# Kernel optimization log

Measured on AMD Instinct MI355X. Metric: run time of the kernel, lower is better.

## Reference

```python
import jax, jax.numpy as jnp
import numpy as np

EPS_LN = 1e-5   # torch.nn.LayerNorm default eps
EPS_Q = 1e-5    # BitNetQuantizer eps
QMAX = 127.0    # 2**(8-1) - 1 for 8-bit activations


def _layernorm(v):
    # LayerNorm without affine params, biased variance (torch default)
    mu = jnp.mean(v, axis=-1, keepdims=True)
    var = jnp.var(v, axis=-1, keepdims=True)
    return (v - mu) / jnp.sqrt(var + EPS_LN)


def setup_inputs() -> dict:
    key = jax.random.key(0)
    k1, k2, k3 = jax.random.split(key, 3)
    B, S, DIN, DOUT = 4, 4096, 2048, 2048
    x = jax.random.normal(k1, (B, S, DIN), dtype=jnp.float32)
    # ternary weights in {-1, 0, +1}
    weight_ternary = jax.random.randint(k2, (DOUT, DIN), -1, 2, dtype=jnp.int32)
    # positive per-row scale (from_float uses a scalar expanded; per-row is the stored form)
    weight_scale = jax.random.uniform(k3, (DOUT,), dtype=jnp.float32, minval=0.01, maxval=0.05)
    return {"x": x, "weight_ternary": weight_ternary, "weight_scale": weight_scale}


def reference(x, weight_ternary, weight_scale):
    # input LayerNorm (no affine)
    xn = _layernorm(x)
    # 8-bit activation quantization: per-token absmax scale
    x_scale = jnp.clip(jnp.max(jnp.abs(xn), axis=-1, keepdims=True), EPS_Q, None) / QMAX
    x_quant = jnp.clip(jnp.round(xn / x_scale), -QMAX, QMAX)
    x_float = x_quant * x_scale  # [B, S, DIN]
    # dequantize ternary weights: [DOUT, DIN]
    w = weight_ternary.astype(jnp.float32) * weight_scale[:, None]
    # F.linear: x @ w.T
    out = jnp.einsum('bsi,oi->bso', x_float, w)
    # output LayerNorm (no affine)
    return _layernorm(out)
```

## Files before the change

kernel.cpp:

```cpp
#include <hip/hip_runtime.h>
#include <hip/hip_bf16.h>
#include <stdint.h>

using int32x4 = __attribute__((ext_vector_type(4))) int;

#define DIN 2048
#define DOUT 2048
#define NTOK 16384
#define KDIM 2048
#define NDIM 2048

#define BM 256
#define BN 256
#define BKB 128
#define NKT (KDIM / BKB)

typedef const __attribute__((address_space(1))) void* gp_t;
typedef __attribute__((address_space(3))) void* lp_t;

__device__ __forceinline__ void gload16(const void* g, void* l) {
    __builtin_amdgcn_global_load_lds((gp_t)g, (lp_t)l, 16, 0, 0);
}

__global__ __launch_bounds__(256) void k_wconv(const int* __restrict__ wt,
                                               signed char* __restrict__ w8) {
    int i = blockIdx.x * 256 + threadIdx.x;
    int4 v = ((const int4*)wt)[i];
    char4 c;
    c.x = (signed char)v.x; c.y = (signed char)v.y;
    c.z = (signed char)v.z; c.w = (signed char)v.w;
    ((char4*)w8)[i] = c;
}

__global__ __launch_bounds__(256) void k_lnq(const float* __restrict__ x,
                                             signed char* __restrict__ xq,
                                             float* __restrict__ xscale) {
    __shared__ float sm[12];
    const int row = blockIdx.x;
    const int tid = threadIdx.x;
    const float* p = x + (size_t)row * DIN;
    const float4 v0 = ((const float4*)p)[tid * 2];
    const float4 v1 = ((const float4*)p)[tid * 2 + 1];
    float vv[8] = {v0.x, v0.y, v0.z, v0.w, v1.x, v1.y, v1.z, v1.w};
    float s = 0.f, ss = 0.f;
#pragma unroll
    for (int i = 0; i < 8; i++) { s += vv[i]; ss += vv[i] * vv[i]; }
#pragma unroll
    for (int o = 32; o; o >>= 1) { s += __shfl_down(s, o); ss += __shfl_down(ss, o); }
    const int wv = tid >> 6;
    if ((tid & 63) == 0) { sm[wv] = s; sm[4 + wv] = ss; }
    __syncthreads();
    s = sm[0] + sm[1] + sm[2] + sm[3];
    ss = sm[4] + sm[5] + sm[6] + sm[7];
    const float mu = s * (1.f / DIN);
    const float var = ss * (1.f / DIN) - mu * mu;
    const float rstd = 1.f / sqrtf(var + 1e-5f);
    float am = 0.f;
#pragma unroll
    for (int i = 0; i < 8; i++) am = fmaxf(am, fabsf(vv[i] - mu));
#pragma unroll
    for (int o = 32; o; o >>= 1) am = fmaxf(am, __shfl_down(am, o));
    __syncthreads();
    if ((tid & 63) == 0) sm[8 + wv] = am;
    __syncthreads();
    am = fmaxf(fmaxf(sm[8], sm[9]), fmaxf(sm[10], sm[11]));
    const float scale = fmaxf(am * rstd, 1e-5f) * (1.f / 127.f);
    union { signed char c[8]; int2 v; } u;
#pragma unroll
    for (int i = 0; i < 8; i++) {
        float xn = (vv[i] - mu) * rstd;
        float t = rintf(xn / scale);
        t = fminf(127.f, fmaxf(-127.f, t));
        u.c[i] = (signed char)t;
    }
    ((int2*)(xq + (size_t)row * DIN))[tid] = u.v;
    if (tid == 0) xscale[row] = scale;
}

#define MFMA4(I, AF) \
    acc[I][0] = __builtin_amdgcn_mfma_i32_16x16x64_i8(AF, b0, acc[I][0], 0, 0, 0); \
    acc[I][1] = __builtin_amdgcn_mfma_i32_16x16x64_i8(AF, b1, acc[I][1], 0, 0, 0); \
    acc[I][2] = __builtin_amdgcn_mfma_i32_16x16x64_i8(AF, b2, acc[I][2], 0, 0, 0); \
    acc[I][3] = __builtin_amdgcn_mfma_i32_16x16x64_i8(AF, b3, acc[I][3], 0, 0, 0);

#define SCHED __builtin_amdgcn_sched_barrier(0);
#define BAR   __builtin_amdgcn_s_barrier();
#define LGKM0 asm volatile("s_waitcnt lgkmcnt(0)" ::: "memory");
#define VM0   asm volatile("s_waitcnt vmcnt(0)" ::: "memory");

__global__ __launch_bounds__(512, 2) void k_gemm(const signed char* __restrict__ A,
                                                 const signed char* __restrict__ B,
                                                 const float* __restrict__ xs,
                                                 const float* __restrict__ wsc,
                                                 float* __restrict__ C) {
    __shared__ __align__(16) signed char lA[2][BM * BKB];
    __shared__ __align__(16) signed char lB[2][BN * BKB];
    __shared__ float s_xs[BM];
    __shared__ float s_ws[BN];

    const int tid = threadIdx.x;
    const int orig = blockIdx.x;
    const int bid = (orig & 7) * 64 + (orig >> 3);
    const int bm = bid >> 3;
    const int bn = bid & 7;

    const int lane = tid & 63;
    const int wave = tid >> 6;
    const int wm = wave >> 2;
    const int wn = wave & 3;
    const int lo = lane & 15;
    const int q  = lane >> 4;

    const int srow = tid >> 3;
    const int schunk = tid & 7;
    const int gchunk = schunk ^ (srow & 7);
    const signed char* gA = A + (size_t)(bm * BM + srow) * KDIM + gchunk * 16;
    const signed char* gB = B + (size_t)(bn * BN + srow) * KDIM + gchunk * 16;
    const int dst = srow * BKB + schunk * 16;

    const int arow = (wm * 128 + lo) * BKB;
    const int brow = (wn * 64 + lo) * BKB;
    const int ck0 = (q ^ (lane & 7)) * 16;
    const int ck1 = ((4 + q) ^ (lane & 7)) * 16;

    if (tid < 256) s_xs[tid] = xs[bm * BM + tid];
    else           s_ws[tid - 256] = wsc[bn * BN + tid - 256];

    {
        signed char* la0 = &lA[0][0];
        signed char* lb0 = &lB[0][0];
        gload16(gA,                       la0 + dst);
        gload16(gA + (size_t)64  * KDIM,  la0 + dst + 64  * BKB);
        gload16(gA + (size_t)128 * KDIM,  la0 + dst + 128 * BKB);
        gload16(gA + (size_t)192 * KDIM,  la0 + dst + 192 * BKB);
        gload16(gB,                       lb0 + dst);
        gload16(gB + (size_t)64  * KDIM,  lb0 + dst + 64  * BKB);
        gload16(gB + (size_t)128 * KDIM,  lb0 + dst + 128 * BKB);
        gload16(gB + (size_t)192 * KDIM,  lb0 + dst + 192 * BKB);
    }
    VM0 SCHED BAR SCHED

    int32x4 acc[8][4];
#pragma unroll
    for (int i = 0; i < 8; i++)
#pragma unroll
        for (int j = 0; j < 4; j++) {
            int32x4 z = {0, 0, 0, 0};
            acc[i][j] = z;
        }

    for (int kt = 0; kt < NKT; ++kt) {
        signed char* lAc = &lA[kt & 1][0];
        signed char* lBc = &lB[kt & 1][0];
        signed char* lAn = &lA[(kt & 1) ^ 1][0];
        signed char* lBn = &lB[(kt & 1) ^ 1][0];
        const bool pf = (kt + 1 < NKT);
        const int kb = (kt + 1) * BKB;
        int32x4 a0, a1, a2, a3, b0, b1, b2, b3;

        a0 = *(const int32x4*)(lAc + arow + 0 * 2048 + ck0);
        a1 = *(const int32x4*)(lAc + arow + 1 * 2048 + ck0);
        a2 = *(const int32x4*)(lAc + arow + 2 * 2048 + ck0);
        a3 = *(const int32x4*)(lAc + arow + 3 * 2048 + ck0);
        b0 = *(const int32x4*)(lBc + brow + 0 * 2048 + ck0);
        b1 = *(const int32x4*)(lBc + brow + 1 * 2048 + ck0);
        b2 = *(const int32x4*)(lBc + brow + 2 * 2048 + ck0);
        b3 = *(const int32x4*)(lBc + brow + 3 * 2048 + ck0);
        if (pf) {
            gload16(gA + kb,                      lAn + dst);
            gload16(gA + kb + (size_t)64  * KDIM, lAn + dst + 64  * BKB);
            gload16(gA + kb + (size_t)128 * KDIM, lAn + dst + 128 * BKB);
            gload16(gA + kb + (size_t)192 * KDIM, lAn + dst + 192 * BKB);
        }
        SCHED BAR LGKM0 SCHED
        __builtin_amdgcn_s_setprio(1);
        MFMA4(0, a0) MFMA4(1, a1) MFMA4(2, a2) MFMA4(3, a3)
        __builtin_amdgcn_s_setprio(0);
        SCHED BAR SCHED

        a0 = *(const int32x4*)(lAc + arow + 4 * 2048 + ck0);
        a1 = *(const int32x4*)(lAc + arow + 5 * 2048 + ck0);
        a2 = *(const int32x4*)(lAc + arow + 6 * 2048 + ck0);
        a3 = *(const int32x4*)(lAc + arow + 7 * 2048 + ck0);
        if (pf) {
            gload16(gB + kb,                      lBn + dst);
            gload16(gB + kb + (size_t)64  * KDIM, lBn + dst + 64  * BKB);
            gload16(gB + kb + (size_t)128 * KDIM, lBn + dst + 128 * BKB);
            gload16(gB + kb + (size_t)192 * KDIM, lBn + dst + 192 * BKB);
        }
        SCHED BAR LGKM0 SCHED
        __builtin_amdgcn_s_setprio(1);
        MFMA4(4, a0) MFMA4(5, a1) MFMA4(6, a2) MFMA4(7, a3)
        __builtin_amdgcn_s_setprio(0);
        SCHED BAR SCHED

        a0 = *(const int32x4*)(lAc + arow + 0 * 2048 + ck1);
        a1 = *(const int32x4*)(lAc + arow + 1 * 2048 + ck1);
        a2 = *(const int32x4*)(lAc + arow + 2 * 2048 + ck1);
        a3 = *(const int32x4*)(lAc + arow + 3 * 2048 + ck1);
        b0 = *(const int32x4*)(lBc + brow + 0 * 2048 + ck1);
        b1 = *(const int32x4*)(lBc + brow + 1 * 2048 + ck1);
        b2 = *(const int32x4*)(lBc + brow + 2 * 2048 + ck1);
        b3 = *(const int32x4*)(lBc + brow + 3 * 2048 + ck1);
        SCHED BAR LGKM0 SCHED
        __builtin_amdgcn_s_setprio(1);
        MFMA4(0, a0) MFMA4(1, a1) MFMA4(2, a2) MFMA4(3, a3)
        __builtin_amdgcn_s_setprio(0);
        SCHED BAR SCHED

        a0 = *(const int32x4*)(lAc + arow + 4 * 2048 + ck1);
        a1 = *(const int32x4*)(lAc + arow + 5 * 2048 + ck1);
        a2 = *(const int32x4*)(lAc + arow + 6 * 2048 + ck1);
        a3 = *(const int32x4*)(lAc + arow + 7 * 2048 + ck1);
        SCHED BAR LGKM0 SCHED
        __builtin_amdgcn_s_setprio(1);
        MFMA4(4, a0) MFMA4(5, a1) MFMA4(6, a2) MFMA4(7, a3)
        __builtin_amdgcn_s_setprio(0);
        VM0 SCHED BAR SCHED
    }

#pragma unroll
    for (int i = 0; i < 8; ++i) {
#pragma unroll
        for (int j = 0; j < 4; ++j) {
            const int ln = wn * 64 + j * 16 + lo;
            const float wsv = s_ws[ln];
            float* cp = C + (size_t)(bm * BM + wm * 128 + i * 16 + q * 4) * NDIM + bn * BN + ln;
#pragma unroll
            for (int r = 0; r < 4; ++r) {
                const int lm = wm * 128 + i * 16 + q * 4 + r;
                cp[(size_t)r * NDIM] = (float)acc[i][j][r] * s_xs[lm] * wsv;
            }
        }
    }
}

__global__ __launch_bounds__(256) void k_lnout(float* __restrict__ y) {
    __shared__ float sm[8];
    const int row = blockIdx.x;
    const int tid = threadIdx.x;
    float* p = y + (size_t)row * DOUT;
    float4 v0 = ((float4*)p)[tid * 2];
    float4 v1 = ((float4*)p)[tid * 2 + 1];
    float vv[8] = {v0.x, v0.y, v0.z, v0.w, v1.x, v1.y, v1.z, v1.w};
    float s = 0.f, ss = 0.f;
#pragma unroll
    for (int i = 0; i < 8; i++) { s += vv[i]; ss += vv[i] * vv[i]; }
#pragma unroll
    for (int o = 32; o; o >>= 1) { s += __shfl_down(s, o); ss += __shfl_down(ss, o); }
    const int wv = tid >> 6;
    if ((tid & 63) == 0) { sm[wv] = s; sm[4 + wv] = ss; }
    __syncthreads();
    s = sm[0] + sm[1] + sm[2] + sm[3];
    ss = sm[4] + sm[5] + sm[6] + sm[7];
    const float mu = s * (1.f / DOUT);
    const float var = ss * (1.f / DOUT) - mu * mu;
    const float rstd = 1.f / sqrtf(var + 1e-5f);
#pragma unroll
    for (int i = 0; i < 8; i++) vv[i] = (vv[i] - mu) * rstd;
    float4 o0, o1;
    o0.x = vv[0]; o0.y = vv[1]; o0.z = vv[2]; o0.w = vv[3];
    o1.x = vv[4]; o1.y = vv[5]; o1.z = vv[6]; o1.w = vv[7];
    ((float4*)p)[tid * 2] = o0;
    ((float4*)p)[tid * 2 + 1] = o1;
}

extern "C" void kernel_launch(void* const* d_in, const int* in_sizes, int n_in,
                              void* d_out, int out_size, void* d_ws, size_t ws_size,
                              hipStream_t stream) {
    const float* x = (const float*)d_in[0];
    const int* wt = (const int*)d_in[1];
    const float* wscale = (const float*)d_in[2];
    float* out = (float*)d_out;

    signed char* w8 = (signed char*)d_ws;
    signed char* xq = (signed char*)d_ws + (size_t)4 * 1024 * 1024;
    float* xs = (float*)((char*)d_ws + (size_t)36 * 1024 * 1024);

    k_wconv<<<(DOUT * DIN / 4) / 256, 256, 0, stream>>>(wt, w8);
    k_lnq<<<NTOK, 256, 0, stream>>>(x, xq, xs);
    k_gemm<<<(NTOK / BM) * (NDIM / BN), 512, 0, stream>>>(xq, w8, xs, wscale, out);
    k_lnout<<<NTOK, 256, 0, stream>>>(out);
}
```

Baseline: 165.0 us.

## Switch int8 GEMM to 3-stage LDS pipeline with 64-byte K tiles

Halves the K tile to 64 bytes and moves from double to triple buffering in LDS, prefetching two tiles ahead. Each iteration now needs one barrier instead of four, and the 16 MFMAs of the second half overlap the remaining LDS reads through partial lgkmcnt waits. The LDS swizzle is rewritten for the 64-byte row. The change cuts synchronisation and exposed load latency, but there are twice as many iterations and the 64-byte rows may cause more LDS bank conflicts.

Result: faster. 157.9 us (-4.3%).

```diff
diff --git a/kernel.cpp b/kernel.cpp
--- a/kernel.cpp
+++ b/kernel.cpp
@@ -12,8 +12,9 @@
 
 #define BM 256
 #define BN 256
-#define BKB 128
+#define BKB 64
 #define NKT (KDIM / BKB)
+#define TILEB (BM * BKB)
 
 typedef const __attribute__((address_space(1))) void* gp_t;
 typedef __attribute__((address_space(3))) void* lp_t;
@@ -85,16 +86,14 @@
 
 #define SCHED __builtin_amdgcn_sched_barrier(0);
 #define BAR   __builtin_amdgcn_s_barrier();
-#define LGKM0 asm volatile("s_waitcnt lgkmcnt(0)" ::: "memory");
-#define VM0   asm volatile("s_waitcnt vmcnt(0)" ::: "memory");
 
 __global__ __launch_bounds__(512, 2) void k_gemm(const signed char* __restrict__ A,
                                                  const signed char* __restrict__ B,
                                                  const float* __restrict__ xs,
                                                  const float* __restrict__ wsc,
                                                  float* __restrict__ C) {
-    __shared__ __align__(16) signed char lA[2][BM * BKB];
-    __shared__ __align__(16) signed char lB[2][BN * BKB];
+    __shared__ __align__(16) signed char lA[3][TILEB];
+    __shared__ __align__(16) signed char lB[3][TILEB];
     __shared__ float s_xs[BM];
     __shared__ float s_ws[BN];
 
@@ -111,34 +110,30 @@
     const int lo = lane & 15;
     const int q  = lane >> 4;
 
-    const int srow = tid >> 3;
-    const int schunk = tid & 7;
-    const int gchunk = schunk ^ (srow & 7);
-    const signed char* gA = A + (size_t)(bm * BM + srow) * KDIM + gchunk * 16;
-    const signed char* gB = B + (size_t)(bn * BN + srow) * KDIM + gchunk * 16;
-    const int dst = srow * BKB + schunk * 16;
-
-    const int arow = (wm * 128 + lo) * BKB;
-    const int brow = (wn * 64 + lo) * BKB;
-    const int ck0 = (q ^ (lane & 7)) * 16;
-    const int ck1 = ((4 + q) ^ (lane & 7)) * 16;
+    const int srow = tid >> 2;
+    const int gch  = (tid & 3) ^ ((srow >> 1) & 3);
+    const signed char* gA = A + (size_t)(bm * BM + srow) * KDIM + gch * 16;
+    const signed char* gB = B + (size_t)(bn * BN + srow) * KDIM + gch * 16;
+    const int dst = tid * 16;
+
+    const int slot = (q ^ ((lo >> 1) & 3)) * 16;
+    const int abase = (wm * 128 + lo) * BKB + slot;
+    const int bbase = (wn * 64 + lo) * BKB + slot;
 
     if (tid < 256) s_xs[tid] = xs[bm * BM + tid];
     else           s_ws[tid - 256] = wsc[bn * BN + tid - 256];
 
-    {
-        signed char* la0 = &lA[0][0];
-        signed char* lb0 = &lB[0][0];
-        gload16(gA,                       la0 + dst);
-        gload16(gA + (size_t)64  * KDIM,  la0 + dst + 64  * BKB);
-        gload16(gA + (size_t)128 * KDIM,  la0 + dst + 128 * BKB);
-        gload16(gA + (size_t)192 * KDIM,  la0 + dst + 192 * BKB);
-        gload16(gB,                       lb0 + dst);
-        gload16(gB + (size_t)64  * KDIM,  lb0 + dst + 64  * BKB);
-        gload16(gB + (size_t)128 * KDIM,  lb0 + dst + 128 * BKB);
-        gload16(gB + (size_t)192 * KDIM,  lb0 + dst + 192 * BKB);
-    }
-    VM0 SCHED BAR SCHED
+#define STAGE_A(T, BUF) \
+    gload16(gA + (T) * BKB,                        &lA[BUF][0] + dst); \
+    gload16(gA + (T) * BKB + (size_t)128 * KDIM,   &lA[BUF][0] + dst + 8192);
+#define STAGE_B(T, BUF) \
+    gload16(gB + (T) * BKB,                        &lB[BUF][0] + dst); \
+    gload16(gB + (T) * BKB + (size_t)128 * KDIM,   &lB[BUF][0] + dst + 8192);
+
+    STAGE_A(0, 0) STAGE_B(0, 0)
+    STAGE_A(1, 1) STAGE_B(1, 1)
+    asm volatile("s_waitcnt vmcnt(0)" ::: "memory");
+    SCHED BAR SCHED
 
     int32x4 acc[8][4];
 #pragma unroll
@@ -149,74 +144,48 @@
             acc[i][j] = z;
         }
 
-    for (int kt = 0; kt < NKT; ++kt) {
-        signed char* lAc = &lA[kt & 1][0];
-        signed char* lBc = &lB[kt & 1][0];
-        signed char* lAn = &lA[(kt & 1) ^ 1][0];
-        signed char* lBn = &lB[(kt & 1) ^ 1][0];
-        const bool pf = (kt + 1 < NKT);
-        const int kb = (kt + 1) * BKB;
-        int32x4 a0, a1, a2, a3, b0, b1, b2, b3;
-
-        a0 = *(const int32x4*)(lAc + arow + 0 * 2048 + ck0);
-        a1 = *(const int32x4*)(lAc + arow + 1 * 2048 + ck0);
-        a2 = *(const int32x4*)(lAc + arow + 2 * 2048 + ck0);
-        a3 = *(const int32x4*)(lAc + arow + 3 * 2048 + ck0);
-        b0 = *(const int32x4*)(lBc + brow + 0 * 2048 + ck0);
-        b1 = *(const int32x4*)(lBc + brow + 1 * 2048 + ck0);
-        b2 = *(const int32x4*)(lBc + brow + 2 * 2048 + ck0);
-        b3 = *(const int32x4*)(lBc + brow + 3 * 2048 + ck0);
-        if (pf) {
-            gload16(gA + kb,                      lAn + dst);
-            gload16(gA + kb + (size_t)64  * KDIM, lAn + dst + 64  * BKB);
-            gload16(gA + kb + (size_t)128 * KDIM, lAn + dst + 128 * BKB);
-            gload16(gA + kb + (size_t)192 * KDIM, lAn + dst + 192 * BKB);
+    int cur = 0, nx2 = 2;
+    for (int t = 0; t < NKT; ++t) {
+        const signed char* lAc = &lA[cur][0];
+        const signed char* lBc = &lB[cur][0];
+        int32x4 a0, a1, a2, a3, a4, a5, a6, a7, b0, b1, b2, b3;
+
+        a0 = *(const int32x4*)(lAc + abase + 0 * 1024);
+        a1 = *(const int32x4*)(lAc + abase + 1 * 1024);
+        a2 = *(const int32x4*)(lAc + abase + 2 * 1024);
+        a3 = *(const int32x4*)(lAc + abase + 3 * 1024);
+        b0 = *(const int32x4*)(lBc + bbase + 0 * 1024);
+        b1 = *(const int32x4*)(lBc + bbase + 1 * 1024);
+        b2 = *(const int32x4*)(lBc + bbase + 2 * 1024);
+        b3 = *(const int32x4*)(lBc + bbase + 3 * 1024);
+        a4 = *(const int32x4*)(lAc + abase + 4 * 1024);
+        a5 = *(const int32x4*)(lAc + abase + 5 * 1024);
+        a6 = *(const int32x4*)(lAc + abase + 6 * 1024);
+        a7 = *(const int32x4*)(lAc + abase + 7 * 1024);
+        asm volatile("s_waitcnt vmcnt(0)" ::: "memory");
+        SCHED
+        BAR
+        SCHED
+        if (t + 2 < NKT) {
+            STAGE_A(t + 2, nx2)
+            STAGE_B(t + 2, nx2)
         }
-        SCHED BAR LGKM0 SCHED
+        SCHED
+        asm volatile("s_waitcnt lgkmcnt(4)" ::: "memory");
+        SCHED
         __builtin_amdgcn_s_setprio(1);
         MFMA4(0, a0) MFMA4(1, a1) MFMA4(2, a2) MFMA4(3, a3)
         __builtin_amdgcn_s_setprio(0);
-        SCHED BAR SCHED
-
-        a0 = *(const int32x4*)(lAc + arow + 4 * 2048 + ck0);
-        a1 = *(const int32x4*)(lAc + arow + 5 * 2048 + ck0);
-        a2 = *(const int32x4*)(lAc + arow + 6 * 2048 + ck0);
-        a3 = *(const int32x4*)(lAc + arow + 7 * 2048 + ck0);
-        if (pf) {
-            gload16(gB + kb,                      lBn + dst);
-            gload16(gB + kb + (size_t)64  * KDIM, lBn + dst + 64  * BKB);
-            gload16(gB + kb + (size_t)128 * KDIM, lBn + dst + 128 * BKB);
-            gload16(gB + kb + (size_t)192 * KDIM, lBn + dst + 192 * BKB);
-        }
-        SCHED BAR LGKM0 SCHED
+        SCHED
+        asm volatile("s_waitcnt lgkmcnt(0)" ::: "memory");
+        SCHED
         __builtin_amdgcn_s_setprio(1);
-        MFMA4(4, a0) MFMA4(5, a1) MFMA4(6, a2) MFMA4(7, a3)
+        MFMA4(4, a4) MFMA4(5, a5) MFMA4(6, a6) MFMA4(7, a7)
         __builtin_amdgcn_s_setprio(0);
-        SCHED BAR SCHED
-
-        a0 = *(const int32x4*)(lAc + arow + 0 * 2048 + ck1);
-        a1 = *(const int32x4*)(lAc + arow + 1 * 2048 + ck1);
-        a2 = *(const int32x4*)(lAc + arow + 2 * 2048 + ck1);
-        a3 = *(const int32x4*)(lAc + arow + 3 * 2048 + ck1);
-        b0 = *(const int32x4*)(lBc + brow + 0 * 2048 + ck1);
-        b1 = *(const int32x4*)(lBc + brow + 1 * 2048 + ck1);
-        b2 = *(const int32x4*)(lBc + brow + 2 * 2048 + ck1);
-        b3 = *(const int32x4*)(lBc + brow + 3 * 2048 + ck1);
-        SCHED BAR LGKM0 SCHED
-        __builtin_amdgcn_s_setprio(1);
-        MFMA4(0, a0) MFMA4(1, a1) MFMA4(2, a2) MFMA4(3, a3)
-        __builtin_amdgcn_s_setprio(0);
-        SCHED BAR SCHED
-
-        a0 = *(const int32x4*)(lAc + arow + 4 * 2048 + ck1);
-        a1 = *(const int32x4*)(lAc + arow + 5 * 2048 + ck1);
-        a2 = *(const int32x4*)(lAc + arow + 6 * 2048 + ck1);
-        a3 = *(const int32x4*)(lAc + arow + 7 * 2048 + ck1);
-        SCHED BAR LGKM0 SCHED
-        __builtin_amdgcn_s_setprio(1);
-        MFMA4(4, a0) MFMA4(5, a1) MFMA4(6, a2) MFMA4(7, a3)
-        __builtin_amdgcn_s_setprio(0);
-        VM0 SCHED BAR SCHED
+        SCHED
+
+        cur = (cur == 2) ? 0 : cur + 1;
+        nx2 = (nx2 == 2) ? 0 : nx2 + 1;
     }
 
 #pragma unroll
```
